# Optimization experiments

Measured on AMD Instinct MI355X. Metric: run time of the kernel, lower is better.

Reference implementation:

```python
import jax, jax.numpy as jnp
import numpy as np

EMB = 64
NODE_DIM = 5
T = 5
B, N = 8, 512


def setup_inputs() -> dict:
    key = jax.random.key(0)
    ks = jax.random.split(key, 24)
    def w(k, shape):
        return jax.random.normal(k, shape, dtype=jnp.float32) * 0.1
    xv = jax.random.normal(ks[0], (B, N, NODE_DIM), dtype=jnp.float32)
    Ws = jax.random.uniform(ks[1], (B, N, N), dtype=jnp.float32)
    reach = jax.random.bernoulli(ks[2], 0.5, (B, N))
    reach = reach.at[:, 0].set(True)  # guarantee at least one reachable node
    return {
        'xv': xv, 'Ws': Ws, 'reachable_nodes': reach,
        'W1a': w(ks[3], (NODE_DIM, EMB)), 'b1a': w(ks[4], (EMB,)),
        'W1b': w(ks[5], (EMB, EMB)),      'b1b': w(ks[6], (EMB,)),
        'W2':  w(ks[7], (EMB, EMB)),      'b2':  w(ks[8], (EMB,)),
        'W3':  w(ks[9], (EMB, EMB)),      'b3':  w(ks[10], (EMB,)),
        'w4':  w(ks[11], (EMB,)),         'b4':  w(ks[12], (EMB,)),
        'W6':  w(ks[13], (EMB, EMB)),     'b6':  w(ks[14], (EMB,)),
        'W7':  w(ks[15], (EMB, EMB)),     'b7':  w(ks[16], (EMB,)),
        'W51': w(ks[17], (2 * EMB, EMB)), 'b51': w(ks[18], (EMB,)),
        'w52': w(ks[19], (EMB,)),         'b52': w(ks[20], ()),
    }


def _struc2vec(xv, Ws, W1a, b1a, W1b, b1b, W2, b2, W3, b3, w4, b4):
    # s1: per-node feature embedding [B,N,E]
    s1 = jax.nn.relu(xv @ W1a + b1a) @ W1b + b1b
    # edge-feature path: relu(theta4(Ws[...,None])) summed over dim 1 -> [B,N,E]
    s3_1 = jax.nn.relu(Ws[..., None] * w4 + b4)  # [B,N,N,E]
    s3 = jnp.sum(s3_1, axis=1) @ W3 + b3         # [B,N,E]
    mu = jnp.zeros(s1.shape, dtype=s1.dtype)
    for _ in range(T):
        s2 = jnp.einsum('bnm,bme->bne', Ws, mu) @ W2 + b2
        mu = jax.nn.relu(s1 + s2 + s3)
    return mu


def reference(xv, Ws, reachable_nodes, W1a, b1a, W1b, b1b, W2, b2, W3, b3,
              w4, b4, W6, b6, W7, b7, W51, b51, w52, b52):
    mu = _struc2vec(xv, Ws, W1a, b1a, W1b, b1b, W2, b2, W3, b3, w4, b4)
    # global state broadcast to every node + local per-node action embedding
    global_state = jnp.sum(mu, axis=1, keepdims=True) @ W6 + b6  # [B,1,E]
    global_state = jnp.broadcast_to(global_state, mu.shape)      # [B,N,E]
    local_action = mu @ W7 + b7                                  # [B,N,E]
    rep = jax.nn.relu(jnp.concatenate([global_state, local_action], axis=2))
    rep = jax.nn.relu(rep) @ W51 + b51                           # relu(relu(.)) as in source
    prob_logits = rep @ w52 + b52                                # [B,N]
    prob_logits = jnp.where(reachable_nodes, prob_logits, -jnp.inf)
    return prob_logits
```

## Files before the change

### kernel.cpp

```cpp
#include <hip/hip_runtime.h>
#include <hip/hip_bf16.h>
#include <cstdint>
#include <cstddef>

#define BB 8
#define NN 512
#define EE 64

typedef __attribute__((ext_vector_type(8))) short short8v;
typedef __attribute__((ext_vector_type(4))) float f32x4;
typedef __attribute__((ext_vector_type(4))) unsigned int u32x4;
typedef __attribute__((ext_vector_type(2))) unsigned int u32x2;

static __device__ __forceinline__ unsigned short f2bf(float f) {
  __hip_bfloat16 h = __float2bfloat16(f);
  return *reinterpret_cast<unsigned short*>(&h);
}
static __device__ __forceinline__ u32x4 ld_b128_sc(const void* p) {
  u32x4 v;
  asm volatile("global_load_dwordx4 %0, %1, off sc0 sc1"
               : "=v"(v) : "v"(p) : "memory");
  return v;
}
static __device__ __forceinline__ unsigned ld_b32_sc(const void* p) {
  unsigned v;
  asm volatile("global_load_dword %0, %1, off sc0 sc1\n\ts_waitcnt vmcnt(0)"
               : "=v"(v) : "v"(p) : "memory");
  return v;
}
static __device__ __forceinline__ void st_b64_sc(void* p, u32x2 v) {
  asm volatile("global_store_dwordx2 %0, %1, off sc0 sc1"
               :: "v"(p), "v"(v) : "memory");
}
static __device__ __forceinline__ void st_b32_sc(void* p, unsigned v) {
  asm volatile("global_store_dword %0, %1, off sc0 sc1"
               :: "v"(p), "v"(v) : "memory");
}
static __device__ __forceinline__ void vm0() {
  asm volatile("s_waitcnt vmcnt(0)" ::: "memory");
}
static __device__ __forceinline__ short8v as_s8(u32x4 v) {
  short8v r; __builtin_memcpy(&r, &v, 16); return r;
}

__global__ __launch_bounds__(512) void k_fused(
    const float* __restrict__ Ws, const float* __restrict__ xv,
    const float* __restrict__ W1a, const float* __restrict__ b1a,
    const float* __restrict__ W1b, const float* __restrict__ b1b,
    const float* __restrict__ W2, const float* __restrict__ b2,
    const float* __restrict__ W3, const float* __restrict__ b3,
    const float* __restrict__ w4, const float* __restrict__ b4,
    const float* __restrict__ W6, const float* __restrict__ b6,
    const float* __restrict__ W7, const float* __restrict__ b7,
    const float* __restrict__ W51, const float* __restrict__ b51,
    const float* __restrict__ w52, const float* __restrict__ b52,
    const void* __restrict__ reach, float* __restrict__ out,
    unsigned short* __restrict__ WsBf, unsigned short* __restrict__ zA,
    unsigned short* __restrict__ zB, float* __restrict__ gpart,
    unsigned* __restrict__ flags) {
  const int blk = blockIdx.x;
  const int b = blk >> 5;
  const int stripe = blk & 31;
  const int n0 = stripe << 4;
  const int t = threadIdx.x;

  __shared__ float tile[128][16];
  __shared__ float W2_lds[64][65];
  __shared__ float sp[16][68];
  __shared__ float half_[16][68];
  __shared__ float hh[16][68];
  __shared__ float base_lds[16][68];
  __shared__ float mu_lds[16][72];
  __shared__ float yred[16][68];
  __shared__ unsigned short zbf[64][20];
  __shared__ float gsl[64], gsr[64], v7l[64], w52l[64], pl_lds[16];
  __shared__ float g0c;
  __shared__ int sbig, sflt;

  auto arrive = [&](int idx) {
    vm0();
    __syncthreads();
    if (t == 0) st_b32_sc(&flags[(b * 8 + idx) * 32 + stripe], 1u);
  };
  auto wait = [&](int idx) {
    if (t < 64) {
      const unsigned* fp = &flags[(b * 8 + idx) * 32 + (t & 31)];
      while (true) {
        unsigned v = ld_b32_sc(fp);
        if (__ballot(v != 0u) == ~0ull) break;
        __builtin_amdgcn_s_sleep(1);
      }
    }
    __syncthreads();
  };

  auto publish_z = [&](unsigned short* dst) {
#pragma unroll
    for (int p = 0; p < 2; ++p) {
      int n = p * 8 + (t >> 6), e = t & 63;
      float z = 0.f;
#pragma unroll 8
      for (int j = 0; j < EE; ++j) z = fmaf(mu_lds[n][j], W2_lds[j][e], z);
      zbf[e][n] = f2bf(z);
    }
    __syncthreads();
    if (t < 256) {
      int e = t >> 2, mq = (t & 3) * 4;
      u32x2 v;
      unsigned short* pv = (unsigned short*)&v;
      pv[0] = zbf[e][mq]; pv[1] = zbf[e][mq + 1];
      pv[2] = zbf[e][mq + 2]; pv[3] = zbf[e][mq + 3];
      st_b64_sc(dst + ((size_t)b * EE + e) * NN + n0 + mq, v);
    }
  };

  const float* wsbase = Ws + (size_t)b * NN * NN;
  const int lrow = t >> 2, lc4 = (t & 3) * 4;
  float4 tr0 = *(const float4*)&wsbase[(size_t)(0 * 128 + lrow) * NN + n0 + lc4];
  float4 tr1 = *(const float4*)&wsbase[(size_t)(1 * 128 + lrow) * NN + n0 + lc4];
  float4 tr2 = *(const float4*)&wsbase[(size_t)(2 * 128 + lrow) * NN + n0 + lc4];
  float4 tr3 = *(const float4*)&wsbase[(size_t)(3 * 128 + lrow) * NN + n0 + lc4];
#pragma unroll
  for (int p = 0; p < 4; ++p) {
    int row = p * 4 + (t >> 7);
    int m4 = (t & 127) * 4;
    size_t g = (size_t)(n0 + row) * NN + m4;
    float4 v = *(const float4*)&wsbase[g];
    ushort4 uv;
    uv.x = f2bf(v.x); uv.y = f2bf(v.y); uv.z = f2bf(v.z); uv.w = f2bf(v.w);
    *(ushort4*)&WsBf[(size_t)b * NN * NN + g] = uv;
  }
#pragma unroll
  for (int k = 0; k < 8; ++k) {
    int idx = t + k * 512;
    W2_lds[idx >> 6][idx & 63] = W2[idx];
  }
  {
    int e = t & 63;
#pragma unroll
    for (int p = 0; p < 2; ++p) {
      int rr = p * 8 + (t >> 6);
      const float* x = xv + ((size_t)b * NN + n0 + rr) * 5;
      float h = b1a[e];
      h = fmaf(x[0], W1a[0 * EE + e], h);
      h = fmaf(x[1], W1a[1 * EE + e], h);
      h = fmaf(x[2], W1a[2 * EE + e], h);
      h = fmaf(x[3], W1a[3 * EE + e], h);
      h = fmaf(x[4], W1a[4 * EE + e], h);
      hh[rr][e] = fmaxf(h, 0.f);
    }
  }
  {
    int ih = t >> 8;
    int n = (t >> 4) & 15;
    int e0 = (t & 15) * 4;
    float4 w4v = *(const float4*)&w4[e0];
    float4 b4v = *(const float4*)&b4[e0];
    float a0 = 0.f, a1 = 0.f, a2 = 0.f, a3 = 0.f;
    int ib = ih * 64;
#pragma unroll
    for (int c = 0; c < 4; ++c) {
      float4 tv = (c == 0) ? tr0 : (c == 1) ? tr1 : (c == 2) ? tr2 : tr3;
      *(float4*)&tile[lrow][lc4] = tv;
      __syncthreads();
#pragma unroll 8
      for (int i = 0; i < 64; ++i) {
        float w = tile[ib + i][n];
        a0 += fmaxf(fmaf(w, w4v.x, b4v.x), 0.f);
        a1 += fmaxf(fmaf(w, w4v.y, b4v.y), 0.f);
        a2 += fmaxf(fmaf(w, w4v.z, b4v.z), 0.f);
        a3 += fmaxf(fmaf(w, w4v.w, b4v.w), 0.f);
      }
      __syncthreads();
    }
    if (ih) {
      half_[n][e0] = a0; half_[n][e0 + 1] = a1;
      half_[n][e0 + 2] = a2; half_[n][e0 + 3] = a3;
    }
    __syncthreads();
    if (!ih) {
      sp[n][e0] = a0 + half_[n][e0];
      sp[n][e0 + 1] = a1 + half_[n][e0 + 1];
      sp[n][e0 + 2] = a2 + half_[n][e0 + 2];
      sp[n][e0 + 3] = a3 + half_[n][e0 + 3];
    }
  }
  __syncthreads();
  {
    int e = t & 63;
#pragma unroll
    for (int p = 0; p < 2; ++p) {
      int rr = p * 8 + (t >> 6);
      float s = b1b[e] + b3[e] + b2[e];
#pragma unroll 8
      for (int j = 0; j < EE; ++j)
        s = fmaf(hh[rr][j], W1b[j * EE + e], fmaf(sp[rr][j], W3[j * EE + e], s));
      base_lds[rr][e] = s;
      mu_lds[rr][e] = fmaxf(s, 0.f);
    }
  }
  __syncthreads();
  publish_z(zA);
  arrive(0);

  const int w = t >> 6, eb = w & 3, kh = w >> 2;
  const int l = t & 63, lr = l & 15, hi = l >> 4;
  const int lk = hi * 8, nq = hi * 4;
  const unsigned short* Ap =
      WsBf + ((size_t)b * NN + n0 + lr) * NN + kh * 256 + lk;
  short8v A0 = *(const short8v*)(Ap + 0);
  short8v A1 = *(const short8v*)(Ap + 32);
  short8v A2 = *(const short8v*)(Ap + 64);
  short8v A3 = *(const short8v*)(Ap + 96);
  short8v A4 = *(const short8v*)(Ap + 128);
  short8v A5 = *(const short8v*)(Ap + 160);
  short8v A6 = *(const short8v*)(Ap + 192);
  short8v A7 = *(const short8v*)(Ap + 224);

  auto prop = [&](const unsigned short* zsrc) {
    const unsigned short* Bp =
        zsrc + ((size_t)b * EE + eb * 16 + lr) * NN + kh * 256 + lk;
    u32x4 q0 = ld_b128_sc(Bp + 0);
    u32x4 q1 = ld_b128_sc(Bp + 32);
    u32x4 q2 = ld_b128_sc(Bp + 64);
    u32x4 q3 = ld_b128_sc(Bp + 96);
    u32x4 q4 = ld_b128_sc(Bp + 128);
    u32x4 q5 = ld_b128_sc(Bp + 160);
    u32x4 q6 = ld_b128_sc(Bp + 192);
    u32x4 q7 = ld_b128_sc(Bp + 224);
    vm0();
    __builtin_amdgcn_sched_barrier(0);
    f32x4 acc = {0.f, 0.f, 0.f, 0.f};
    acc = __builtin_amdgcn_mfma_f32_16x16x32_bf16(A0, as_s8(q0), acc, 0, 0, 0);
    acc = __builtin_amdgcn_mfma_f32_16x16x32_bf16(A1, as_s8(q1), acc, 0, 0, 0);
    acc = __builtin_amdgcn_mfma_f32_16x16x32_bf16(A2, as_s8(q2), acc, 0, 0, 0);
    acc = __builtin_amdgcn_mfma_f32_16x16x32_bf16(A3, as_s8(q3), acc, 0, 0, 0);
    acc = __builtin_amdgcn_mfma_f32_16x16x32_bf16(A4, as_s8(q4), acc, 0, 0, 0);
    acc = __builtin_amdgcn_mfma_f32_16x16x32_bf16(A5, as_s8(q5), acc, 0, 0, 0);
    acc = __builtin_amdgcn_mfma_f32_16x16x32_bf16(A6, as_s8(q6), acc, 0, 0, 0);
    acc = __builtin_amdgcn_mfma_f32_16x16x32_bf16(A7, as_s8(q7), acc, 0, 0, 0);
    if (kh == 1) {
#pragma unroll
      for (int q = 0; q < 4; ++q) yred[nq + q][eb * 16 + lr] = acc[q];
    }
    __syncthreads();
    if (kh == 0) {
#pragma unroll
      for (int q = 0; q < 4; ++q) {
        int ep = eb * 16 + lr;
        mu_lds[nq + q][ep] =
            fmaxf(base_lds[nq + q][ep] + acc[q] + yred[nq + q][ep], 0.f);
      }
    }
    __syncthreads();
  };

  wait(0);
  prop(zA); publish_z(zB); arrive(1); wait(1);
  prop(zB); publish_z(zA); arrive(2); wait(2);
  prop(zA); publish_z(zB); arrive(3); wait(3);
  prop(zB);

  if (t < 64) {
    float s = 0.f;
#pragma unroll
    for (int n = 0; n < 16; ++n) s += mu_lds[n][t];
    st_b32_sc(&gpart[((size_t)b * 32 + stripe) * EE + t], __float_as_uint(s));
  }
  arrive(4);

  if (t == 0) { sbig = 0; sflt = 0; }
  if (t < 64) w52l[t] = w52[t];
  __syncthreads();
  if (t < 256) {
    const unsigned int* rw = (const unsigned int*)reach;
    bool big = false, flt = false;
#pragma unroll
    for (int l2 = 0; l2 < 4; ++l2) {
      unsigned int v = rw[t + l2 * 256];
      if (v > 1u) big = true;
      if (v == 0x3f800000u) flt = true;
    }
    if (big) sbig = 1;
    if (flt) sflt = 1;
  }
  if (t >= 320 && t < 384) {
    int j = t - 320;
    float v = 0.f;
#pragma unroll 8
    for (int e = 0; e < EE; ++e) v = fmaf(W51[(EE + j) * EE + e], w52[e], v);
    v7l[j] = v;
  }
  __syncthreads();
#pragma unroll
  for (int p = 0; p < 2; ++p) {
    int n = p * 8 + (t >> 6), e7 = t & 63;
    float la = b7[e7];
#pragma unroll 8
    for (int e = 0; e < EE; ++e) la = fmaf(mu_lds[n][e], W7[e * EE + e7], la);
    float c = fmaxf(la, 0.f) * v7l[e7];
#pragma unroll
    for (int off = 32; off > 0; off >>= 1) c += __shfl_down(c, off, 64);
    if (e7 == 0) pl_lds[n] = c;
  }

  wait(4);

  float* gacc = &tile[0][0];
  {
    int s = t >> 4, e4 = (t & 15) * 4;
    u32x4 v = ld_b128_sc(&gpart[((size_t)b * 32 + s) * EE + e4]);
    vm0();
    gacc[s * EE + e4 + 0] = __uint_as_float(v.x);
    gacc[s * EE + e4 + 1] = __uint_as_float(v.y);
    gacc[s * EE + e4 + 2] = __uint_as_float(v.z);
    gacc[s * EE + e4 + 3] = __uint_as_float(v.w);
  }
  __syncthreads();
  if (t < 64) {
    float s = 0.f;
#pragma unroll 8
    for (int k = 0; k < 32; ++k) s += gacc[k * EE + t];
    gsl[t] = s;
  }
  __syncthreads();
  if (t < 64) {
    float a = b6[t];
#pragma unroll 8
    for (int k = 0; k < EE; ++k) a = fmaf(gsl[k], W6[k * EE + t], a);
    gsr[t] = fmaxf(a, 0.f);
  }
  __syncthreads();
  if (t < 64) {
    float q = 0.f;
#pragma unroll 8
    for (int j = 0; j < EE; ++j) q = fmaf(gsr[j], W51[j * EE + t], q);
    float pg = (q + b51[t]) * w52l[t];
#pragma unroll
    for (int off = 32; off > 0; off >>= 1) pg += __shfl_down(pg, off, 64);
    if (t == 0) g0c = pg + b52[0];
  }
  __syncthreads();
  if (t < 16) {
    int row = b * NN + n0 + t;
    bool rc;
    if (sflt)      rc = ((const float*)reach)[row] != 0.f;
    else if (sbig) rc = ((const unsigned char*)reach)[row] != 0;
    else           rc = ((const int*)reach)[row] != 0;
    out[row] = rc ? (pl_lds[t] + g0c) : -1.0e30f;
  }
}

extern "C" void kernel_launch(void* const* d_in, const int* in_sizes, int n_in,
                              void* d_out, int out_size, void* d_ws, size_t ws_size,
                              hipStream_t stream) {
  const float* xv  = (const float*)d_in[0];
  const float* Ws  = (const float*)d_in[1];
  const void*  rch = d_in[2];
  const float* W1a = (const float*)d_in[3];
  const float* b1a = (const float*)d_in[4];
  const float* W1b = (const float*)d_in[5];
  const float* b1b = (const float*)d_in[6];
  const float* W2  = (const float*)d_in[7];
  const float* b2  = (const float*)d_in[8];
  const float* W3  = (const float*)d_in[9];
  const float* b3  = (const float*)d_in[10];
  const float* w4  = (const float*)d_in[11];
  const float* b4  = (const float*)d_in[12];
  const float* W6  = (const float*)d_in[13];
  const float* b6  = (const float*)d_in[14];
  const float* W7  = (const float*)d_in[15];
  const float* b7  = (const float*)d_in[16];
  const float* W51 = (const float*)d_in[17];
  const float* b51 = (const float*)d_in[18];
  const float* w52 = (const float*)d_in[19];
  const float* b52 = (const float*)d_in[20];
  float* out = (float*)d_out;

  char* wsb = (char*)d_ws;
  unsigned short* WsBf = (unsigned short*)wsb;
  unsigned short* zA   = (unsigned short*)(wsb + (4096 << 10));
  unsigned short* zB   = (unsigned short*)(wsb + (4608 << 10));
  float* gpart         = (float*)(wsb + (5120 << 10));
  unsigned* flags      = (unsigned*)(wsb + (5184 << 10));

  hipMemsetAsync((void*)flags, 0, 8192, stream);
  k_fused<<<dim3(256), dim3(512), 0, stream>>>(
      Ws, xv, W1a, b1a, W1b, b1b, W2, b2, W3, b3, w4, b4,
      W6, b6, W7, b7, W51, b51, w52, b52, rch, out,
      WsBf, zA, zB, gpart, flags);
}
```

Measured before the change: 62.98 us.

## Use MFMA for mu@W2, drop bf16 Ws workspace copy, keep mu in bf16 LDS

Replaces the scalar FP32 mu@W2 loop with two bf16 MFMA 16x16x32 ops per wave, with W2 held in registers as bf16 fragments. It removes the bf16 copy of Ws written to global memory and instead converts the A fragments straight from the fp32 Ws rows into registers. The mu state is now kept in LDS as bf16 in MFMA-friendly layout, and the s3 tile is transposed so it can be read with float4 loads. This cuts global write traffic and ALU work, but adds bf16 rounding to mu, which is now also used for the global sum and the W7 path.

```diff
diff --git a/kernel.cpp b/kernel.cpp
--- a/kernel.cpp
+++ b/kernel.cpp
@@ -15,6 +15,10 @@
 static __device__ __forceinline__ unsigned short f2bf(float f) {
   __hip_bfloat16 h = __float2bfloat16(f);
   return *reinterpret_cast<unsigned short*>(&h);
+}
+static __device__ __forceinline__ float bf2f(unsigned short u) {
+  unsigned x = ((unsigned)u) << 16;
+  float f; __builtin_memcpy(&f, &x, 4); return f;
 }
 static __device__ __forceinline__ u32x4 ld_b128_sc(const void* p) {
   u32x4 v;
@@ -55,24 +59,25 @@
     const float* __restrict__ W51, const float* __restrict__ b51,
     const float* __restrict__ w52, const float* __restrict__ b52,
     const void* __restrict__ reach, float* __restrict__ out,
-    unsigned short* __restrict__ WsBf, unsigned short* __restrict__ zA,
-    unsigned short* __restrict__ zB, float* __restrict__ gpart,
-    unsigned* __restrict__ flags) {
+    unsigned short* __restrict__ zA, unsigned short* __restrict__ zB,
+    float* __restrict__ gpart, unsigned* __restrict__ flags) {
   const int blk = blockIdx.x;
   const int b = blk >> 5;
   const int stripe = blk & 31;
   const int n0 = stripe << 4;
   const int t = threadIdx.x;
-
-  __shared__ float tile[128][16];
-  __shared__ float W2_lds[64][65];
+  const int w = t >> 6, l = t & 63, lr = l & 15, hi = l >> 4;
+  const int lk = hi * 8, nq = hi * 4, eb = w & 3, kh = w >> 2;
+
+  __shared__ __attribute__((aligned(16))) float tileT[16][132];
   __shared__ float sp[16][68];
   __shared__ float half_[16][68];
   __shared__ float hh[16][68];
   __shared__ float base_lds[16][68];
-  __shared__ float mu_lds[16][72];
   __shared__ float yred[16][68];
-  __shared__ unsigned short zbf[64][20];
+  __shared__ __attribute__((aligned(16))) unsigned short muzA[512];
+  __shared__ __attribute__((aligned(16))) unsigned short muzB[512];
+  __shared__ __attribute__((aligned(16))) unsigned short zbf[64][20];
   __shared__ float gsl[64], gsr[64], v7l[64], w52l[64], pl_lds[16];
   __shared__ float g0c;
   __shared__ int sbig, sflt;
@@ -94,24 +99,10 @@
     __syncthreads();
   };
 
-  auto publish_z = [&](unsigned short* dst) {
-#pragma unroll
-    for (int p = 0; p < 2; ++p) {
-      int n = p * 8 + (t >> 6), e = t & 63;
-      float z = 0.f;
-#pragma unroll 8
-      for (int j = 0; j < EE; ++j) z = fmaf(mu_lds[n][j], W2_lds[j][e], z);
-      zbf[e][n] = f2bf(z);
-    }
-    __syncthreads();
-    if (t < 256) {
-      int e = t >> 2, mq = (t & 3) * 4;
-      u32x2 v;
-      unsigned short* pv = (unsigned short*)&v;
-      pv[0] = zbf[e][mq]; pv[1] = zbf[e][mq + 1];
-      pv[2] = zbf[e][mq + 2]; pv[3] = zbf[e][mq + 3];
-      st_b64_sc(dst + ((size_t)b * EE + e) * NN + n0 + mq, v);
-    }
+  auto muz_store = [&](int node, int e, float v) {
+    int eh = e & 31;
+    unsigned short* dst = (e < 32) ? muzA : muzB;
+    dst[((eh >> 3) * 16 + node) * 8 + (eh & 7)] = f2bf(v);
   };
 
   const float* wsbase = Ws + (size_t)b * NN * NN;
@@ -120,21 +111,18 @@
   float4 tr1 = *(const float4*)&wsbase[(size_t)(1 * 128 + lrow) * NN + n0 + lc4];
   float4 tr2 = *(const float4*)&wsbase[(size_t)(2 * 128 + lrow) * NN + n0 + lc4];
   float4 tr3 = *(const float4*)&wsbase[(size_t)(3 * 128 + lrow) * NN + n0 + lc4];
-#pragma unroll
-  for (int p = 0; p < 4; ++p) {
-    int row = p * 4 + (t >> 7);
-    int m4 = (t & 127) * 4;
-    size_t g = (size_t)(n0 + row) * NN + m4;
-    float4 v = *(const float4*)&wsbase[g];
-    ushort4 uv;
-    uv.x = f2bf(v.x); uv.y = f2bf(v.y); uv.z = f2bf(v.z); uv.w = f2bf(v.w);
-    *(ushort4*)&WsBf[(size_t)b * NN * NN + g] = uv;
-  }
-#pragma unroll
-  for (int k = 0; k < 8; ++k) {
-    int idx = t + k * 512;
-    W2_lds[idx >> 6][idx & 63] = W2[idx];
-  }
+
+  short8v WBa = {}, WBb = {};
+  if (w < 4) {
+    union { unsigned short u[8]; short8v v; } pa, pb;
+#pragma unroll
+    for (int j = 0; j < 8; ++j) {
+      pa.u[j] = f2bf(W2[(8 * hi + j) * EE + 16 * w + lr]);
+      pb.u[j] = f2bf(W2[(8 * hi + j + 32) * EE + 16 * w + lr]);
+    }
+    WBa = pa.v; WBb = pb.v;
+  }
+
   {
     int e = t & 63;
 #pragma unroll
@@ -161,15 +149,22 @@
 #pragma unroll
     for (int c = 0; c < 4; ++c) {
       float4 tv = (c == 0) ? tr0 : (c == 1) ? tr1 : (c == 2) ? tr2 : tr3;
-      *(float4*)&tile[lrow][lc4] = tv;
+      tileT[lc4 + 0][lrow] = tv.x;
+      tileT[lc4 + 1][lrow] = tv.y;
+      tileT[lc4 + 2][lrow] = tv.z;
+      tileT[lc4 + 3][lrow] = tv.w;
       __syncthreads();
-#pragma unroll 8
-      for (int i = 0; i < 64; ++i) {
-        float w = tile[ib + i][n];
-        a0 += fmaxf(fmaf(w, w4v.x, b4v.x), 0.f);
-        a1 += fmaxf(fmaf(w, w4v.y, b4v.y), 0.f);
-        a2 += fmaxf(fmaf(w, w4v.z, b4v.z), 0.f);
-        a3 += fmaxf(fmaf(w, w4v.w, b4v.w), 0.f);
+#pragma unroll
+      for (int i4 = 0; i4 < 16; ++i4) {
+        float4 wv = *(const float4*)&tileT[n][ib + i4 * 4];
+#pragma unroll
+        for (int k = 0; k < 4; ++k) {
+          float ww = (k == 0) ? wv.x : (k == 1) ? wv.y : (k == 2) ? wv.z : wv.w;
+          a0 += fmaxf(fmaf(ww, w4v.x, b4v.x), 0.f);
+          a1 += fmaxf(fmaf(ww, w4v.y, b4v.y), 0.f);
+          a2 += fmaxf(fmaf(ww, w4v.z, b4v.z), 0.f);
+          a3 += fmaxf(fmaf(ww, w4v.w, b4v.w), 0.f);
+        }
       }
       __syncthreads();
     }
@@ -179,7 +174,7 @@
     }
     __syncthreads();
     if (!ih) {
-      sp[n][e0] = a0 + half_[n][e0];
+      sp[n][e0]     = a0 + half_[n][e0];
       sp[n][e0 + 1] = a1 + half_[n][e0 + 1];
       sp[n][e0 + 2] = a2 + half_[n][e0 + 2];
       sp[n][e0 + 3] = a3 + half_[n][e0 + 3];
@@ -196,26 +191,54 @@
       for (int j = 0; j < EE; ++j)
         s = fmaf(hh[rr][j], W1b[j * EE + e], fmaf(sp[rr][j], W3[j * EE + e], s));
       base_lds[rr][e] = s;
-      mu_lds[rr][e] = fmaxf(s, 0.f);
-    }
-  }
-  __syncthreads();
-  publish_z(zA);
+      muz_store(rr, e, fmaxf(s, 0.f));
+    }
+  }
+  __syncthreads();
+
+  auto zphase = [&]() {
+    if (w < 4) {
+      short8v a0 = *(const short8v*)&muzA[l * 8];
+      short8v a1 = *(const short8v*)&muzB[l * 8];
+      f32x4 zacc = {0.f, 0.f, 0.f, 0.f};
+      zacc = __builtin_amdgcn_mfma_f32_16x16x32_bf16(a0, WBa, zacc, 0, 0, 0);
+      zacc = __builtin_amdgcn_mfma_f32_16x16x32_bf16(a1, WBb, zacc, 0, 0, 0);
+      ushort4 u;
+      u.x = f2bf(zacc[0]); u.y = f2bf(zacc[1]);
+      u.z = f2bf(zacc[2]); u.w = f2bf(zacc[3]);
+      *(ushort4*)&zbf[16 * w + lr][4 * hi] = u;
+    }
+  };
+  auto publish = [&](unsigned short* dst) {
+    if (t < 256) {
+      int e = t >> 2, mq = (t & 3) * 4;
+      u32x2 v;
+      __builtin_memcpy(&v, &zbf[e][mq], 8);
+      st_b64_sc(dst + ((size_t)b * EE + e) * NN + n0 + mq, v);
+    }
+  };
+
+  zphase();
+  __syncthreads();
+  publish(zA);
   arrive(0);
 
-  const int w = t >> 6, eb = w & 3, kh = w >> 2;
-  const int l = t & 63, lr = l & 15, hi = l >> 4;
-  const int lk = hi * 8, nq = hi * 4;
-  const unsigned short* Ap =
-      WsBf + ((size_t)b * NN + n0 + lr) * NN + kh * 256 + lk;
-  short8v A0 = *(const short8v*)(Ap + 0);
-  short8v A1 = *(const short8v*)(Ap + 32);
-  short8v A2 = *(const short8v*)(Ap + 64);
-  short8v A3 = *(const short8v*)(Ap + 96);
-  short8v A4 = *(const short8v*)(Ap + 128);
-  short8v A5 = *(const short8v*)(Ap + 160);
-  short8v A6 = *(const short8v*)(Ap + 192);
-  short8v A7 = *(const short8v*)(Ap + 224);
+  short8v A0, A1, A2, A3, A4, A5, A6, A7;
+  {
+    const float* arow = wsbase + (size_t)(n0 + lr) * NN + kh * 256 + lk;
+    union { unsigned short u[8]; short8v v; } pk;
+#define LDA(DST, OFF)                                                        \
+    { float4 fa = *(const float4*)(arow + OFF);                              \
+      float4 fb = *(const float4*)(arow + OFF + 4);                          \
+      pk.u[0] = f2bf(fa.x); pk.u[1] = f2bf(fa.y);                            \
+      pk.u[2] = f2bf(fa.z); pk.u[3] = f2bf(fa.w);                            \
+      pk.u[4] = f2bf(fb.x); pk.u[5] = f2bf(fb.y);                            \
+      pk.u[6] = f2bf(fb.z); pk.u[7] = f2bf(fb.w);                            \
+      DST = pk.v; }
+    LDA(A0, 0)   LDA(A1, 32)  LDA(A2, 64)  LDA(A3, 96)
+    LDA(A4, 128) LDA(A5, 160) LDA(A6, 192) LDA(A7, 224)
+#undef LDA
+  }
 
   auto prop = [&](const unsigned short* zsrc) {
     const unsigned short* Bp =
@@ -245,26 +268,28 @@
     }
     __syncthreads();
     if (kh == 0) {
+      int ep = eb * 16 + lr;
 #pragma unroll
       for (int q = 0; q < 4; ++q) {
-        int ep = eb * 16 + lr;
-        mu_lds[nq + q][ep] =
-            fmaxf(base_lds[nq + q][ep] + acc[q] + yred[nq + q][ep], 0.f);
+        float v = fmaxf(base_lds[nq + q][ep] + acc[q] + yred[nq + q][ep], 0.f);
+        muz_store(nq + q, ep, v);
       }
     }
     __syncthreads();
   };
 
   wait(0);
-  prop(zA); publish_z(zB); arrive(1); wait(1);
-  prop(zB); publish_z(zA); arrive(2); wait(2);
-  prop(zA); publish_z(zB); arrive(3); wait(3);
+  prop(zA); zphase(); __syncthreads(); publish(zB); arrive(1); wait(1);
+  prop(zB); zphase(); __syncthreads(); publish(zA); arrive(2); wait(2);
+  prop(zA); zphase(); __syncthreads(); publish(zB); arrive(3); wait(3);
   prop(zB);
 
   if (t < 64) {
+    int eh = t & 31, jj = t & 7, lb = (eh >> 3) * 16;
+    const unsigned short* dst = (t < 32) ? muzA : muzB;
     float s = 0.f;
 #pragma unroll
-    for (int n = 0; n < 16; ++n) s += mu_lds[n][t];
+    for (int n = 0; n < 16; ++n) s += bf2f(dst[(lb + n) * 8 + jj]);
     st_b32_sc(&gpart[((size_t)b * 32 + stripe) * EE + t], __float_as_uint(s));
   }
   arrive(4);
@@ -296,8 +321,18 @@
   for (int p = 0; p < 2; ++p) {
     int n = p * 8 + (t >> 6), e7 = t & 63;
     float la = b7[e7];
-#pragma unroll 8
-    for (int e = 0; e < EE; ++e) la = fmaf(mu_lds[n][e], W7[e * EE + e7], la);
+#pragma unroll
+    for (int h = 0; h < 2; ++h) {
+      const unsigned short* dst = h ? muzB : muzA;
+#pragma unroll
+      for (int h2 = 0; h2 < 4; ++h2) {
+        short8v mv = *(const short8v*)&dst[(h2 * 16 + n) * 8];
+#pragma unroll
+        for (int j = 0; j < 8; ++j)
+          la = fmaf(bf2f((unsigned short)mv[j]),
+                    W7[(h * 32 + h2 * 8 + j) * EE + e7], la);
+      }
+    }
     float c = fmaxf(la, 0.f) * v7l[e7];
 #pragma unroll
     for (int off = 32; off > 0; off >>= 1) c += __shfl_down(c, off, 64);
@@ -306,7 +341,7 @@
 
   wait(4);
 
-  float* gacc = &tile[0][0];
+  float* gacc = &tileT[0][0];
   {
     int s = t >> 4, e4 = (t & 15) * 4;
     u32x4 v = ld_b128_sc(&gpart[((size_t)b * 32 + s) * EE + e4]);
@@ -378,15 +413,14 @@
   float* out = (float*)d_out;
 
   char* wsb = (char*)d_ws;
-  unsigned short* WsBf = (unsigned short*)wsb;
-  unsigned short* zA   = (unsigned short*)(wsb + (4096 << 10));
-  unsigned short* zB   = (unsigned short*)(wsb + (4608 << 10));
-  float* gpart         = (float*)(wsb + (5120 << 10));
-  unsigned* flags      = (unsigned*)(wsb + (5184 << 10));
+  unsigned short* zA   = (unsigned short*)wsb;
+  unsigned short* zB   = (unsigned short*)(wsb + (512 << 10));
+  float* gpart         = (float*)(wsb + (1024 << 10));
+  unsigned* flags      = (unsigned*)(wsb + (1088 << 10));
 
   hipMemsetAsync((void*)flags, 0, 8192, stream);
   k_fused<<<dim3(256), dim3(512), 0, stream>>>(
       Ws, xv, W1a, b1a, W1b, b1b, W2, b2, W3, b3, w4, b4,
       W6, b6, W7, b7, W51, b51, w52, b52, rch, out,
-      WsBf, zA, zB, gpart, flags);
-}
+      zA, zB, gpart, flags);
+}
```

After: 56.55 us. 10.2% less time.
